# Kernel tuning notes

Measured on AMD Instinct MI355X. Metric: run time of the kernel, lower is better.

Reference implementation:

```python
import jax, jax.numpy as jnp
import numpy as np
from jax import lax

B, L, E = 2, 2048, 1024          # batch, seq_len, embed_dim
NL = 2                            # n_layers
DI = 2 * E                        # d_inner (expand=2)
DS = 16                           # d_state
DC = 4                            # d_conv
DTR = (E + 15) // 16              # dt_rank = ceil(d_model/16) = 64


def setup_inputs() -> dict:
    key = jax.random.key(0)
    ks = jax.random.split(key, 12)
    s = 0.02
    inp = {
        "x": jax.random.normal(ks[0], (B, L, E), jnp.float32),
        "pos_embed": jax.random.normal(ks[1], (L, E), jnp.float32) * s,
        "in_proj_w": jax.random.normal(ks[2], (NL, 2 * DI, E), jnp.float32) * s,
        "conv_w": jax.random.normal(ks[3], (NL, DI, DC), jnp.float32) * s,
        "conv_b": jnp.zeros((NL, DI), jnp.float32),
        "x_proj_w": jax.random.normal(ks[4], (NL, DTR + 2 * DS, DI), jnp.float32) * s,
        "dt_proj_w": jax.random.normal(ks[5], (NL, DI, DTR), jnp.float32) * s,
        "dt_bias": jax.random.normal(ks[6], (NL, DI), jnp.float32) * 0.1,
        "A_log": jnp.broadcast_to(jnp.log(jnp.arange(1, DS + 1, dtype=jnp.float32)), (NL, DI, DS)) + 0.0,
        "D_skip": jnp.ones((NL, DI), jnp.float32),
        "out_proj_w": jax.random.normal(ks[7], (NL, E, DI), jnp.float32) * s,
        "norm_w": jnp.ones((NL, E), jnp.float32),
    }
    return inp


def _rmsnorm(x, w, eps=1e-6):
    return x * lax.rsqrt(jnp.mean(x * x, axis=-1, keepdims=True) + eps) * w


def _mamba(h, in_w, cw, cb, xw, dtw, dtb, A_log, Dp, ow):
    # h: (B, L, E)
    xz = jnp.einsum("ble,de->bld", h, in_w)          # (B, L, 2*DI)
    xc, z = jnp.split(xz, 2, axis=-1)                 # each (B, L, DI)
    # causal depthwise conv1d (kernel DC)
    xp = jnp.pad(xc, ((0, 0), (DC - 1, 0), (0, 0)))
    xconv = cb
    acc = jnp.zeros_like(xc)
    for k in range(DC):
        acc = acc + cw[:, k] * xp[:, k:k + xc.shape[1], :]
    xc = jax.nn.silu(acc + cb)
    # input-dependent SSM params
    x_dbl = jnp.einsum("bld,rd->blr", xc, xw)         # (B, L, DTR+2*DS)
    dt, Bm, C = jnp.split(x_dbl, [DTR, DTR + DS], axis=-1)
    delta = jax.nn.softplus(jnp.einsum("blr,dr->bld", dt, dtw) + dtb)  # (B, L, DI)
    A = -jnp.exp(A_log)                               # (DI, DS)

    def step(hst, inp):
        d, bm, c, u = inp                             # (B,DI),(B,DS),(B,DS),(B,DI)
        hst = jnp.exp(d[..., None] * A) * hst + (d * u)[..., None] * bm[:, None, :]
        y = jnp.einsum("bdn,bn->bd", hst, c)
        return hst, y

    h0 = jnp.zeros((h.shape[0], DI, DS), h.dtype)
    _, ys = lax.scan(step, h0, (delta.swapaxes(0, 1), Bm.swapaxes(0, 1),
                                C.swapaxes(0, 1), xc.swapaxes(0, 1)))
    y = ys.swapaxes(0, 1) + xc * Dp                   # (B, L, DI)
    y = y * jax.nn.silu(z)
    return jnp.einsum("bld,ed->ble", y, ow)


def reference(x, pos_embed, in_proj_w, conv_w, conv_b, x_proj_w, dt_proj_w,
              dt_bias, A_log, D_skip, out_proj_w, norm_w):
    h = x + pos_embed[None, :x.shape[1]]
    for i in range(in_proj_w.shape[0]):
        y = _mamba(h, in_proj_w[i], conv_w[i], conv_b[i], x_proj_w[i],
                   dt_proj_w[i], dt_bias[i], A_log[i], D_skip[i], out_proj_w[i])
        h = _rmsnorm(y + h, norm_w[i])
    return h
```

## Files before the change

### kernel.cpp

```cpp
#include <hip/hip_runtime.h>

#define B_   2
#define L_   2048
#define E_   1024
#define NL_  2
#define DI_  2048
#define DS_  16
#define DC_  4
#define DTR_ 64
#define NXD_ 96
#define M_   (B_ * L_)
#define NCH_ 64
#define LC_  32

typedef __attribute__((ext_vector_type(8))) short bf16x8;
typedef __attribute__((ext_vector_type(4))) float f32x4;

__device__ __forceinline__ float bf2f(unsigned short u) {
    return __uint_as_float(((unsigned)u) << 16);
}
__device__ __forceinline__ unsigned short f2bf(float f) {
    unsigned u = __float_as_uint(f);
    u += 0x7fff + ((u >> 16) & 1);
    return (unsigned short)(u >> 16);
}

#define LOG2E_ 1.44269504f
#define LN2_   0.69314718f

__device__ __forceinline__ float sigmoidf_(float x) {
    return __builtin_amdgcn_rcpf(1.f + __builtin_amdgcn_exp2f(-x * LOG2E_));
}
__device__ __forceinline__ float softplusf_(float x) {
    float e = __builtin_amdgcn_exp2f(x * LOG2E_);
    float s = LN2_ * __builtin_amdgcn_logf(1.f + e);
    return x > 15.f ? x : s;
}
__device__ __forceinline__ float expf_(float x) {
    return __builtin_amdgcn_exp2f(x * LOG2E_);
}
__device__ __forceinline__ float ldin(const void* p, size_t i, int isbf) {
    return isbf ? bf2f(((const unsigned short*)p)[i]) : ((const float*)p)[i];
}
__device__ __forceinline__ void gld_lds16(const unsigned short* g, unsigned short* l) {
    __builtin_amdgcn_global_load_lds(
        (const __attribute__((address_space(1))) unsigned int*)g,
        (__attribute__((address_space(3))) unsigned int*)l, 16, 0, 0);
}

__device__ __forceinline__ void expvec(int fast, float dv, const float* a2, float* e) {
    if (fast) {
        float p1 = __builtin_amdgcn_exp2f(dv * a2[0]);
        float p2 = p1 * p1, p4 = p2 * p2, p8 = p4 * p4;
        e[0] = p1;        e[1] = p2;        e[2] = p2 * p1;   e[3] = p4;
        e[4] = p4 * p1;   e[5] = p4 * p2;   e[6] = e[5] * p1; e[7] = p8;
        e[8] = p8 * p1;   e[9] = p8 * p2;   e[10] = e[9] * p1; e[11] = p8 * p4;
        e[12] = e[11] * p1; e[13] = e[11] * p2; e[14] = e[13] * p1; e[15] = p8 * p8;
    } else {
#pragma unroll
        for (int n = 0; n < 16; ++n) e[n] = __builtin_amdgcn_exp2f(dv * a2[n]);
    }
}

__global__ __launch_bounds__(256) void detect_kernel(const unsigned* __restrict__ x,
                                                     int* __restrict__ flags)
{
    __shared__ int cnt;
    if (threadIdx.x == 0) cnt = 0;
    __syncthreads();
    unsigned v = x[threadIdx.x];
    int e = (v >> 7) & 0xFF;
    if (e >= 90 && e <= 140) atomicAdd(&cnt, 1);
    __syncthreads();
    if (threadIdx.x == 0) {
        flags[0] = (cnt >= 192) ? 1 : 0;
        flags[1] = 1;
        flags[2] = 1;
    }
}

__global__ __launch_bounds__(256) void chk_alog(
    const void* __restrict__ alog, int* __restrict__ flags)
{
    int isbf = flags[0];
    int i = blockIdx.x * 256 + threadIdx.x;
    int layer = i / (DI_ * DS_);
    int n = i & (DS_ - 1);
    float a  = -expf_(ldin(alog, i, isbf));
    float a0 = -expf_(ldin(alog, i - n, isbf));
    float want = (n + 1) * a0;
    if (fabsf(a - want) > 0.02f * fabsf(want))
        atomicAnd(&flags[1 + layer], 0);
}

#define WB_IN_  0
#define WB_XW_  4194304
#define WB_DTW_ 4456448
#define WB_OW_  4587520
#define WB_TOT_ 6684672
__global__ __launch_bounds__(256) void cvt_layer_kernel(
    const void* __restrict__ inw, const void* __restrict__ xw,
    const void* __restrict__ dtw, const void* __restrict__ ow,
    int layer, unsigned short* __restrict__ wbuf, const int* __restrict__ flag)
{
    int isbf = *flag;
    int i = blockIdx.x * 256 + threadIdx.x;
    unsigned short v;
    if (i < WB_XW_) {
        v = isbf ? ((const unsigned short*)inw)[(size_t)layer * 2 * DI_ * E_ + i]
                 : f2bf(((const float*)inw)[(size_t)layer * 2 * DI_ * E_ + i]);
    } else if (i < WB_DTW_) {
        int j = i - WB_XW_; int r = j >> 11, k = j & (DI_ - 1);
        v = (r < NXD_)
          ? (isbf ? ((const unsigned short*)xw)[(size_t)layer * NXD_ * DI_ + (size_t)r * DI_ + k]
                  : f2bf(((const float*)xw)[(size_t)layer * NXD_ * DI_ + (size_t)r * DI_ + k]))
          : (unsigned short)0;
    } else if (i < WB_OW_) {
        int j = i - WB_DTW_;
        v = isbf ? ((const unsigned short*)dtw)[(size_t)layer * DI_ * DTR_ + j]
                 : f2bf(((const float*)dtw)[(size_t)layer * DI_ * DTR_ + j]);
    } else {
        int j = i - WB_OW_;
        v = isbf ? ((const unsigned short*)ow)[(size_t)layer * E_ * DI_ + j]
                 : f2bf(((const float*)ow)[(size_t)layer * E_ * DI_ + j]);
    }
    wbuf[i] = v;
}

__global__ __launch_bounds__(256) void add_pos_kernel(
    const void* __restrict__ x, const void* __restrict__ pos,
    float* __restrict__ h, unsigned short* __restrict__ h16,
    const int* __restrict__ flag)
{
    int isbf = *flag;
    int i = blockIdx.x * 256 + threadIdx.x;
    float v = ldin(x, i, isbf) + ldin(pos, i & (L_ * E_ - 1), isbf);
    h[i] = v;
    h16[i] = f2bf(v);
}

__global__ __launch_bounds__(256) void gemm_mfma(
    const unsigned short* __restrict__ A, int lda,
    const unsigned short* __restrict__ W, int ldw,
    void* __restrict__ C, int ldc, int Ksplit, size_t cSliceStride,
    const void* __restrict__ bias, size_t boff,
    void* __restrict__ C2, int ep, const int* __restrict__ flag)
{
    __shared__ unsigned short As[128 * 64];
    __shared__ unsigned short Bs[128 * 64];
    int tid = threadIdx.x;
    int lane = tid & 63, w = tid >> 6;
    int m0 = blockIdx.x * 128, n0 = blockIdx.y * 128;
    int wm = (w >> 1) * 64, wn = (w & 1) * 64;
    int col = lane & 15, quad = lane >> 4;
    int kstart = blockIdx.z * Ksplit;

    f32x4 acc[4][4];
#pragma unroll
    for (int i = 0; i < 4; ++i)
#pragma unroll
        for (int j = 0; j < 4; ++j)
            acc[i][j] = (f32x4){0.f, 0.f, 0.f, 0.f};

    for (int kt = kstart; kt < kstart + Ksplit; kt += 64) {
#pragma unroll
        for (int i = 0; i < 4; ++i) {
            int seg = i * 4 + w;
            int q = seg * 64 + lane;
            int r = q >> 3, cd = q & 7;
            int cs = cd ^ (r & 7);
            gld_lds16(A + (size_t)(m0 + r) * lda + kt + cs * 8, &As[seg * 512]);
            gld_lds16(W + (size_t)(n0 + r) * ldw + kt + cs * 8, &Bs[seg * 512]);
        }
        __syncthreads();
#pragma unroll
        for (int ks = 0; ks < 2; ++ks) {
            bf16x8 af[4], bfr[4];
#pragma unroll
            for (int t = 0; t < 4; ++t) {
                int rowA = wm + t * 16 + col;
                int ca = ks * 4 + quad;
                af[t]  = *(const bf16x8*)&As[rowA * 64 + ((ca ^ (rowA & 7)) * 8)];
                int rowB = wn + t * 16 + col;
                bfr[t] = *(const bf16x8*)&Bs[rowB * 64 + ((ca ^ (rowB & 7)) * 8)];
            }
#pragma unroll
            for (int tm = 0; tm < 4; ++tm)
#pragma unroll
                for (int tn = 0; tn < 4; ++tn)
                    acc[tm][tn] = __builtin_amdgcn_mfma_f32_16x16x32_bf16(
                        af[tm], bfr[tn], acc[tm][tn], 0, 0, 0);
        }
        __syncthreads();
    }

    int isbf = flag ? *flag : 1;
    float* Cp = (float*)C + (size_t)blockIdx.z * cSliceStride;
#pragma unroll
    for (int tm = 0; tm < 4; ++tm)
#pragma unroll
        for (int tn = 0; tn < 4; ++tn)
#pragma unroll
            for (int rg = 0; rg < 4; ++rg) {
                int gm = m0 + wm + tm * 16 + quad * 4 + rg;
                int gn = n0 + wn + tn * 16 + col;
                float v = acc[tm][tn][rg];
                if (ep == 0) {
                    Cp[(size_t)gm * ldc + gn] = v;
                } else {
                    v = softplusf_(v + ldin(bias, boff + gn, isbf));
                    ((unsigned short*)C)[(size_t)gm * ldc + gn] = f2bf(v);
                }
            }
}

#define G8_NT (E_ / 32)
__global__ __launch_bounds__(512) void gemm_inproj8(
    const unsigned short* __restrict__ A,
    const unsigned short* __restrict__ W,
    unsigned short* __restrict__ Cx,
    unsigned short* __restrict__ Cz)
{
    __shared__ unsigned short lds[65536];
    int tid = threadIdx.x;
    int lane = tid & 63, w = tid >> 6;
    int wr = w >> 2, wc = w & 3;
    int col = lane & 15, quad = lane >> 4;

    int flat = blockIdx.y * 16 + blockIdx.x;
    int nn = (flat & 7) * 32 + (flat >> 3);
    int cch = nn >> 5, wi = nn & 31;
    int bx = (cch & 3) * 4 + (wi & 3);
    int by = (cch >> 2) * 8 + (wi >> 2);
    int m0 = bx * 256, n0 = by * 256;

    const unsigned short* srcA = A + (size_t)(m0 + (lane & 15)) * E_ + (lane >> 4) * 8;
    const unsigned short* srcW = W + (size_t)(n0 + (lane & 15)) * E_ + (lane >> 4) * 8;

    f32x4 acc[8][4];
#pragma unroll
    for (int i = 0; i < 8; ++i)
#pragma unroll
        for (int j = 0; j < 4; ++j)
            acc[i][j] = (f32x4){0.f, 0.f, 0.f, 0.f};

#pragma unroll
    for (int tp = 0; tp < 3; ++tp) {
#pragma unroll
        for (int s = 0; s < 2; ++s) {
            int seg = s * 8 + w;
            gld_lds16(srcA + (size_t)seg * 16 * E_ + tp * 32, &lds[tp * 16384 + seg * 512]);
            gld_lds16(srcW + (size_t)seg * 16 * E_ + tp * 32, &lds[tp * 16384 + 8192 + seg * 512]);
        }
    }

    for (int t = 0; t < G8_NT; ++t) {
        if (t < G8_NT - 2)       asm volatile("s_waitcnt vmcnt(8)" ::: "memory");
        else if (t == G8_NT - 2) asm volatile("s_waitcnt vmcnt(4)" ::: "memory");
        else                     asm volatile("s_waitcnt vmcnt(0)" ::: "memory");
        __builtin_amdgcn_s_barrier();

        int cb = (t & 3) * 16384;
        int sb = ((t + 3) & 3) * 16384;
        int kt = (t + 3) * 32;

        if ((t + 3) < G8_NT) {
#pragma unroll
            for (int s = 0; s < 2; ++s) {
                int seg = s * 8 + w;
                gld_lds16(srcA + (size_t)seg * 16 * E_ + kt, &lds[sb + seg * 512]);
                gld_lds16(srcW + (size_t)seg * 16 * E_ + kt, &lds[sb + 8192 + seg * 512]);
            }
        }

        bf16x8 bfr[4], af[8];
#pragma unroll
        for (int tn = 0; tn < 4; ++tn)
            bfr[tn] = *(const bf16x8*)&lds[cb + 8192 + (wc * 4 + tn) * 512 + quad * 128 + col * 8];
#pragma unroll
        for (int t8 = 0; t8 < 8; ++t8)
            af[t8] = *(const bf16x8*)&lds[cb + (wr * 8 + t8) * 512 + quad * 128 + col * 8];

        __builtin_amdgcn_s_setprio(1);
#pragma unroll
        for (int tm = 0; tm < 8; ++tm)
#pragma unroll
            for (int tn = 0; tn < 4; ++tn)
                acc[tm][tn] = __builtin_amdgcn_mfma_f32_16x16x32_bf16(
                    af[tm], bfr[tn], acc[tm][tn], 0, 0, 0);
        __builtin_amdgcn_s_setprio(0);
    }

    unsigned short* dst = (n0 < DI_) ? Cx : Cz;
    int nb = (n0 < DI_) ? n0 : n0 - DI_;
#pragma unroll
    for (int tm = 0; tm < 8; ++tm)
#pragma unroll
        for (int tn = 0; tn < 4; ++tn)
#pragma unroll
            for (int rg = 0; rg < 4; ++rg) {
                int gm = m0 + wr * 128 + tm * 16 + quad * 4 + rg;
                int gn = nb + wc * 64 + tn * 16 + col;
                dst[(size_t)gm * DI_ + gn] = f2bf(acc[tm][tn][rg]);
            }
}

__global__ __launch_bounds__(256) void xproj_reduce(
    const float* __restrict__ part, float* __restrict__ xdbl,
    unsigned short* __restrict__ dt16)
{
    int i = blockIdx.x * 256 + threadIdx.x;
    int r = i >> 7, c = i & 127;
    float v = 0.f;
#pragma unroll
    for (int s = 0; s < 8; ++s) v += part[(size_t)s * (M_ * 128) + i];
    if (c < NXD_) xdbl[(size_t)r * NXD_ + c] = v;
    if (c < DTR_) dt16[(size_t)r * DTR_ + c] = f2bf(v);
}

__global__ __launch_bounds__(256) void conv_prep(
    const void* __restrict__ cw, size_t cwoff, const void* __restrict__ cb,
    size_t cboff, float* __restrict__ cwT, float* __restrict__ cbF,
    const int* __restrict__ flag)
{
    int isbf = *flag;
    int d = blockIdx.x * 256 + threadIdx.x;
#pragma unroll
    for (int k = 0; k < DC_; ++k)
        cwT[k * DI_ + d] = ldin(cw, cwoff + (size_t)d * DC_ + k, isbf);
    cbF[d] = ldin(cb, cboff + d, isbf);
}

#define CT_ 4
__global__ __launch_bounds__(256) void conv_silu_v(
    const unsigned short* __restrict__ xcr16, const float* __restrict__ cwT,
    const float* __restrict__ cbF, unsigned short* __restrict__ xc16)
{
    int g = blockIdx.x;
    int bl0 = g * CT_;
    int l0 = bl0 & (L_ - 1);
    int d = threadIdx.x * 8;

    float w[DC_][8], bias[8];
#pragma unroll
    for (int k = 0; k < DC_; ++k) {
        *(float4*)&w[k][0] = *(const float4*)&cwT[k * DI_ + d];
        *(float4*)&w[k][4] = *(const float4*)&cwT[k * DI_ + d + 4];
    }
    *(float4*)&bias[0] = *(const float4*)&cbF[d];
    *(float4*)&bias[4] = *(const float4*)&cbF[d + 4];

    float xr[DC_ - 1 + CT_][8];
#pragma unroll
    for (int r = 0; r < DC_ - 1 + CT_; ++r) {
        int l = l0 - (DC_ - 1) + r;
        if (l >= 0) {
            bf16x8 v = *(const bf16x8*)&xcr16[(size_t)(bl0 - (DC_ - 1) + r) * DI_ + d];
#pragma unroll
            for (int j = 0; j < 8; ++j) xr[r][j] = bf2f((unsigned short)v[j]);
        } else {
#pragma unroll
            for (int j = 0; j < 8; ++j) xr[r][j] = 0.f;
        }
    }

#pragma unroll
    for (int t = 0; t < CT_; ++t) {
        float acc[8];
#pragma unroll
        for (int j = 0; j < 8; ++j) acc[j] = bias[j];
#pragma unroll
        for (int k = 0; k < DC_; ++k)
#pragma unroll
            for (int j = 0; j < 8; ++j)
                acc[j] = fmaf(w[k][j], xr[t + k][j], acc[j]);
        bf16x8 ov;
#pragma unroll
        for (int j = 0; j < 8; ++j) {
            float s = acc[j] * sigmoidf_(acc[j]);
            ov[j] = (short)f2bf(s);
        }
        *(bf16x8*)&xc16[(size_t)(bl0 + t) * DI_ + d] = ov;
    }
}

__global__ __launch_bounds__(256) void scan_part1(
    const unsigned short* __restrict__ dl16, const unsigned short* __restrict__ xc16,
    const float* __restrict__ xdbl,
    const void* __restrict__ A_log, size_t aoff,
    float* __restrict__ sumdbuf, float* __restrict__ scrS,
    const int* __restrict__ flags, int layer)
{
    int isbf = flags[0], fast = flags[1 + layer];
    __shared__ float bs[LC_][16];
    int c = blockIdx.y;
    int b = blockIdx.x >> 3;
    int d = ((blockIdx.x & 7) << 8) + threadIdx.x;
    for (int i = threadIdx.x; i < LC_ * 16; i += 256) {
        int l = i >> 4, n = i & 15;
        bs[l][n] = xdbl[((size_t)b * L_ + c * LC_ + l) * NXD_ + DTR_ + n];
    }
    __syncthreads();
    float a2[16];
#pragma unroll
    for (int n = 0; n < 16; ++n)
        a2[n] = -expf_(ldin(A_log, aoff + (size_t)d * DS_ + n, isbf)) * LOG2E_;
    float s[16] = {};
    float sumd = 0.f;
    const unsigned short* dp = dl16 + ((size_t)b * L_ + c * LC_) * DI_ + d;
    const unsigned short* up = xc16 + ((size_t)b * L_ + c * LC_) * DI_ + d;
    for (int l = 0; l < LC_; ++l) {
        float dv = bf2f(dp[(size_t)l * DI_]);
        float u  = bf2f(up[(size_t)l * DI_]);
        sumd += dv;
        float dvu = dv * u;
        float e[16];
        expvec(fast, dv, a2, e);
        float4 b0 = *(const float4*)&bs[l][0];
        float4 b1 = *(const float4*)&bs[l][4];
        float4 b2 = *(const float4*)&bs[l][8];
        float4 b3 = *(const float4*)&bs[l][12];
        float bv[16] = {b0.x,b0.y,b0.z,b0.w, b1.x,b1.y,b1.z,b1.w,
                        b2.x,b2.y,b2.z,b2.w, b3.x,b3.y,b3.z,b3.w};
#pragma unroll
        for (int n = 0; n < 16; ++n)
            s[n] = fmaf(e[n], s[n], dvu * bv[n]);
    }
    int g = b * DI_ + d;
    sumdbuf[(size_t)c * (B_ * DI_) + g] = sumd;
    size_t base = ((size_t)c * (B_ * DI_) + g) * 16;
#pragma unroll
    for (int q = 0; q < 4; ++q)
        *(float4*)&scrS[base + q * 4] =
            make_float4(s[q*4], s[q*4+1], s[q*4+2], s[q*4+3]);
}

__global__ __launch_bounds__(256) void scan_combine(
    const float* __restrict__ sumdbuf, float* __restrict__ scrS,
    const void* __restrict__ A_log, size_t aoff, const int* __restrict__ flags)
{
    int isbf = flags[0];
    int t = blockIdx.x * 256 + threadIdx.x;
    int g = t >> 4, n = t & 15;
    int d = g & (DI_ - 1);
    float a2 = -expf_(ldin(A_log, aoff + (size_t)d * DS_ + n, isbf)) * LOG2E_;
    float sd[NCH_], sl[NCH_];
#pragma unroll
    for (int c = 0; c < NCH_; ++c) {
        sd[c] = sumdbuf[(size_t)c * (B_ * DI_) + g];
        sl[c] = scrS[(size_t)c * (B_ * DI_ * 16) + t];
    }
    float s = 0.f;
#pragma unroll
    for (int c = 0; c < NCH_; ++c) {
        float P = __builtin_amdgcn_exp2f(a2 * sd[c]);
        float nxt = fmaf(P, s, sl[c]);
        scrS[(size_t)c * (B_ * DI_ * 16) + t] = s;
        s = nxt;
    }
}

__global__ __launch_bounds__(256) void scan_part2(
    const unsigned short* __restrict__ dl16, unsigned short* __restrict__ xc16,
    const float* __restrict__ xdbl, const unsigned short* __restrict__ z,
    const void* __restrict__ A_log, size_t aoff,
    const void* __restrict__ Dskip, size_t doff,
    const float* __restrict__ scrS, const int* __restrict__ flags, int layer)
{
    int isbf = flags[0], fast = flags[1 + layer];
    __shared__ float bs[LC_][32];
    int c = blockIdx.y;
    int b = blockIdx.x >> 3;
    int d = ((blockIdx.x & 7) << 8) + threadIdx.x;
    for (int i = threadIdx.x; i < LC_ * 32; i += 256) {
        int l = i >> 5, n = i & 31;
        bs[l][n] = xdbl[((size_t)b * L_ + c * LC_ + l) * NXD_ + DTR_ + n];
    }
    __syncthreads();
    float a2[16];
#pragma unroll
    for (int n = 0; n < 16; ++n)
        a2[n] = -expf_(ldin(A_log, aoff + (size_t)d * DS_ + n, isbf)) * LOG2E_;
    float Dv = ldin(Dskip, doff + d, isbf);
    int g = b * DI_ + d;
    size_t sbase = ((size_t)c * (B_ * DI_) + g) * 16;
    float s[16];
#pragma unroll
    for (int q = 0; q < 4; ++q) {
        float4 sv = *(const float4*)&scrS[sbase + q * 4];
        s[q*4] = sv.x; s[q*4+1] = sv.y; s[q*4+2] = sv.z; s[q*4+3] = sv.w;
    }

    const unsigned short* dp = dl16 + ((size_t)b * L_ + c * LC_) * DI_ + d;
    unsigned short* up = xc16 + ((size_t)b * L_ + c * LC_) * DI_ + d;
    const unsigned short* zp = z + ((size_t)b * L_ + c * LC_) * DI_ + d;
    for (int l = 0; l < LC_; ++l) {
        float dv = bf2f(dp[(size_t)l * DI_]);
        float u  = bf2f(up[(size_t)l * DI_]);
        float dvu = dv * u;
        float e[16];
        expvec(fast, dv, a2, e);
        float4 b0 = *(const float4*)&bs[l][0];
        float4 b1 = *(const float4*)&bs[l][4];
        float4 b2 = *(const float4*)&bs[l][8];
        float4 b3 = *(const float4*)&bs[l][12];
        float4 c0 = *(const float4*)&bs[l][16];
        float4 c1 = *(const float4*)&bs[l][20];
        float4 c2 = *(const float4*)&bs[l][24];
        float4 c3 = *(const float4*)&bs[l][28];
        float bv[16] = {b0.x,b0.y,b0.z,b0.w, b1.x,b1.y,b1.z,b1.w,
                        b2.x,b2.y,b2.z,b2.w, b3.x,b3.y,b3.z,b3.w};
        float cv[16] = {c0.x,c0.y,c0.z,c0.w, c1.x,c1.y,c1.z,c1.w,
                        c2.x,c2.y,c2.z,c2.w, c3.x,c3.y,c3.z,c3.w};
        float y = 0.f;
#pragma unroll
        for (int n = 0; n < 16; ++n) {
            s[n] = fmaf(e[n], s[n], dvu * bv[n]);
            y = fmaf(s[n], cv[n], y);
        }
        float zv = bf2f(zp[(size_t)l * DI_]);
        up[(size_t)l * DI_] = f2bf((y + u * Dv) * (zv * sigmoidf_(zv)));
    }
}

__global__ __launch_bounds__(256) void rmsnorm_kernel(
    const float* __restrict__ y0, const float* __restrict__ y1,
    float* __restrict__ h, unsigned short* __restrict__ h16,
    const void* __restrict__ nw, size_t nwoff, void* __restrict__ out,
    int write_out, const int* __restrict__ flag)
{
    int isbf = *flag;
    __shared__ float red[4];
    int row = blockIdx.x;
    float* hp = h + (size_t)row * E_;
    float v[4]; float ss = 0.f;
#pragma unroll
    for (int i = 0; i < 4; ++i) {
        int e = threadIdx.x + i * 256;
        size_t idx = (size_t)row * E_ + e;
        v[i] = y0[idx] + y1[idx] + hp[e];
        ss += v[i] * v[i];
    }
#pragma unroll
    for (int off = 1; off < 64; off <<= 1) ss += __shfl_xor(ss, off, 64);
    if ((threadIdx.x & 63) == 0) red[threadIdx.x >> 6] = ss;
    __syncthreads();
    ss = red[0] + red[1] + red[2] + red[3];
    float scale = rsqrtf(ss * (1.f / E_) + 1e-6f);
#pragma unroll
    for (int i = 0; i < 4; ++i) {
        int e = threadIdx.x + i * 256;
        float hv = v[i] * scale * ldin(nw, nwoff + e, isbf);
        hp[e] = hv;
        h16[(size_t)row * E_ + e] = f2bf(hv);
        if (write_out) {
            size_t oi = (size_t)row * E_ + e;
            if (isbf) ((unsigned short*)out)[oi] = f2bf(hv);
            else      ((float*)out)[oi] = hv;
        }
    }
}

extern "C" void kernel_launch(void* const* d_in, const int* in_sizes, int n_in,
                              void* d_out, int out_size, void* d_ws, size_t ws_size,
                              hipStream_t stream)
{
    const void* x    = d_in[0];
    const void* pos  = d_in[1];
    const void* inw  = d_in[2];
    const void* cw   = d_in[3];
    const void* cb   = d_in[4];
    const void* xw   = d_in[5];
    const void* dtw  = d_in[6];
    const void* dtb  = d_in[7];
    const void* alog = d_in[8];
    const void* dsk  = d_in[9];
    const void* ow   = d_in[10];
    const void* nw   = d_in[11];

    float* ws = (float*)d_ws;
    float* h      = ws;
    unsigned short* h16  = (unsigned short*)(ws + 4194304);
    unsigned short* z16  = (unsigned short*)(ws + 6291456);
    unsigned short* xc16 = (unsigned short*)(ws + 10485760);
    float* D      = ws + 14680064;
    float* R      = ws + 23068672;
    float* xdbl   = ws + 27262976;
    unsigned short* dt16 = (unsigned short*)(ws + 27656192);
    float* sumd   = ws + 27787264;
    unsigned short* wbuf = (unsigned short*)(ws + 28049408);
    int* flags    = (int*)(ws + 31391744);

    unsigned short* xcr16 = (unsigned short*)R;
    float* xp_part = R;
    float* scrS    = R;
    unsigned short* dl16 = (unsigned short*)D;
    float* yout0 = D;
    float* yout1 = D + (size_t)M_ * E_;
    float* cwT = sumd;
    float* cbF = sumd + DC_ * DI_;

    detect_kernel<<<1, 256, 0, stream>>>((const unsigned*)x, flags);
    chk_alog<<<NL_ * DI_ * DS_ / 256, 256, 0, stream>>>(alog, flags);
    add_pos_kernel<<<M_ * E_ / 256, 256, 0, stream>>>(x, pos, h, h16, flags);

    for (int layer = 0; layer < NL_; ++layer) {
        cvt_layer_kernel<<<WB_TOT_ / 256, 256, 0, stream>>>(
            inw, xw, dtw, ow, layer, wbuf, flags);
        conv_prep<<<DI_ / 256, 256, 0, stream>>>(
            cw, (size_t)layer * DI_ * DC_, cb, (size_t)layer * DI_, cwT, cbF, flags);

        gemm_inproj8<<<dim3(M_ / 256, 2 * DI_ / 256, 1), 512, 0, stream>>>(
            h16, wbuf + WB_IN_, xcr16, z16);
        conv_silu_v<<<M_ / CT_, 256, 0, stream>>>(xcr16, cwT, cbF, xc16);
        gemm_mfma<<<dim3(M_ / 128, 1, 8), 256, 0, stream>>>(
            xc16, DI_, wbuf + WB_XW_, DI_, xp_part, 128, DI_ / 8, (size_t)M_ * 128,
            nullptr, 0, nullptr, 0, flags);
        xproj_reduce<<<M_ * 128 / 256, 256, 0, stream>>>(xp_part, xdbl, dt16);
        gemm_mfma<<<dim3(M_ / 128, DI_ / 128, 1), 256, 0, stream>>>(
            dt16, DTR_, wbuf + WB_DTW_, DTR_, dl16, DI_, DTR_, 0,
            dtb, (size_t)layer * DI_, nullptr, 2, flags);
        scan_part1<<<dim3(B_ * DI_ / 256, NCH_), 256, 0, stream>>>(
            dl16, xc16, xdbl, alog, (size_t)layer * DI_ * DS_, sumd, scrS, flags, layer);
        scan_combine<<<B_ * DI_ * DS_ / 256, 256, 0, stream>>>(
            sumd, scrS, alog, (size_t)layer * DI_ * DS_, flags);
        scan_part2<<<dim3(B_ * DI_ / 256, NCH_), 256, 0, stream>>>(
            dl16, xc16, xdbl, z16, alog, (size_t)layer * DI_ * DS_,
            dsk, (size_t)layer * DI_, scrS, flags, layer);
        gemm_mfma<<<dim3(M_ / 128, E_ / 128, 2), 256, 0, stream>>>(
            xc16, DI_, wbuf + WB_OW_, DI_, yout0, E_, DI_ / 2, (size_t)M_ * E_,
            nullptr, 0, nullptr, 0, flags);
        rmsnorm_kernel<<<M_, 256, 0, stream>>>(
            yout0, yout1, h, h16, nw, (size_t)layer * E_, d_out,
            layer == NL_ - 1 ? 1 : 0, flags);
    }
}
```

Before: 567.6 us.

## Read bf16 weights directly and re-pipeline in-proj GEMM with half-phase staging

When inputs are already bf16, the weight-conversion kernel now skips copying the in_proj, dt_proj and out_proj weights, and the GEMMs read the original weight arrays directly. This removes redundant copy traffic. The in-projection GEMM mainloop is rewritten to use a 64-wide K tile with double-buffered LDS. Each tile is processed in eight phases that interleave inline-asm ds_read_b128 fragment loads, global-to-LDS staging and MFMA bursts, each phase separated by explicit barriers and waitcnts. This aims to overlap memory and compute more finely, at the cost of more barriers and fragile hand-coded wait counts.

```diff
diff --git a/kernel.cpp b/kernel.cpp
--- a/kernel.cpp
+++ b/kernel.cpp
@@ -47,6 +47,11 @@
         (const __attribute__((address_space(1))) unsigned int*)g,
         (__attribute__((address_space(3))) unsigned int*)l, 16, 0, 0);
 }
+__device__ __forceinline__ bf16x8 ds_read128_(unsigned byteoff) {
+    bf16x8 r;
+    asm volatile("ds_read_b128 %0, %1" : "=&v"(r) : "v"(byteoff));
+    return r;
+}
 
 __device__ __forceinline__ void expvec(int fast, float dv, const float* a2, float* e) {
     if (fast) {
@@ -105,6 +110,7 @@
 {
     int isbf = *flag;
     int i = blockIdx.x * 256 + threadIdx.x;
+    if (isbf && (i < WB_XW_ || i >= WB_DTW_)) return;
     unsigned short v;
     if (i < WB_XW_) {
         v = isbf ? ((const unsigned short*)inw)[(size_t)layer * 2 * DI_ * E_ + i]
@@ -144,10 +150,13 @@
     const unsigned short* __restrict__ W, int ldw,
     void* __restrict__ C, int ldc, int Ksplit, size_t cSliceStride,
     const void* __restrict__ bias, size_t boff,
-    void* __restrict__ C2, int ep, const int* __restrict__ flag)
+    void* __restrict__ C2, int ep, const int* __restrict__ flag,
+    const unsigned short* __restrict__ Worig)
 {
     __shared__ unsigned short As[128 * 64];
     __shared__ unsigned short Bs[128 * 64];
+    int isbf = flag ? *flag : 1;
+    const unsigned short* Wp = (Worig && isbf) ? Worig : W;
     int tid = threadIdx.x;
     int lane = tid & 63, w = tid >> 6;
     int m0 = blockIdx.x * 128, n0 = blockIdx.y * 128;
@@ -170,7 +179,7 @@
             int r = q >> 3, cd = q & 7;
             int cs = cd ^ (r & 7);
             gld_lds16(A + (size_t)(m0 + r) * lda + kt + cs * 8, &As[seg * 512]);
-            gld_lds16(W + (size_t)(n0 + r) * ldw + kt + cs * 8, &Bs[seg * 512]);
+            gld_lds16(Wp + (size_t)(n0 + r) * ldw + kt + cs * 8, &Bs[seg * 512]);
         }
         __syncthreads();
 #pragma unroll
@@ -194,7 +203,6 @@
         __syncthreads();
     }
 
-    int isbf = flag ? *flag : 1;
     float* Cp = (float*)C + (size_t)blockIdx.z * cSliceStride;
 #pragma unroll
     for (int tm = 0; tm < 4; ++tm)
@@ -214,14 +222,57 @@
             }
 }
 
-#define G8_NT (E_ / 32)
+template <int KS, int MH, int RB, int CHK>
+__device__ __forceinline__ void g8_phase(
+    unsigned baseA, unsigned baseB,
+    bf16x8 (&af)[4], bf16x8 (&bfr)[4], f32x4 (&acc)[8][4],
+    int doStage, int st_t, int st_isB, int st_ks,
+    const unsigned short* srcA, const unsigned short* srcW,
+    unsigned short* ldsb, int w)
+{
+    if (RB) {
+#pragma unroll
+        for (int j = 0; j < 4; ++j)
+            bfr[j] = ds_read128_(baseB + j * 2048 + KS * 1024);
+    }
+#pragma unroll
+    for (int f = 0; f < 4; ++f)
+        af[f] = ds_read128_(baseA + MH * 8192 + f * 2048 + KS * 1024);
+    if (doStage) {
+        const unsigned short* s0 = (st_isB ? srcW : srcA)
+            + (size_t)w * 16 * E_ + st_t * 64 + st_ks * 32;
+        unsigned short* d0 = ldsb + (st_t & 1) * 32768 + st_isB * 16384
+            + w * 1024 + st_ks * 512;
+        gld_lds16(s0, d0);
+        gld_lds16(s0 + (size_t)8 * 16 * E_, d0 + 8 * 1024);
+    }
+    __builtin_amdgcn_s_barrier();
+    asm volatile("s_waitcnt lgkmcnt(0)" ::: "memory");
+    __builtin_amdgcn_sched_barrier(0);
+    __builtin_amdgcn_s_setprio(1);
+#pragma unroll
+    for (int f = 0; f < 4; ++f)
+#pragma unroll
+        for (int j = 0; j < 4; ++j)
+            acc[MH * 4 + f][j] = __builtin_amdgcn_mfma_f32_16x16x32_bf16(
+                af[f], bfr[j], acc[MH * 4 + f][j], 0, 0, 0);
+    __builtin_amdgcn_s_setprio(0);
+    if (CHK == 8) { asm volatile("s_waitcnt vmcnt(8)" ::: "memory"); __builtin_amdgcn_sched_barrier(0); }
+    if (CHK == 4) { asm volatile("s_waitcnt vmcnt(4)" ::: "memory"); __builtin_amdgcn_sched_barrier(0); }
+    if (CHK == 0) { asm volatile("s_waitcnt vmcnt(0)"  ::: "memory"); __builtin_amdgcn_sched_barrier(0); }
+    __builtin_amdgcn_s_barrier();
+}
+
 __global__ __launch_bounds__(512) void gemm_inproj8(
     const unsigned short* __restrict__ A,
-    const unsigned short* __restrict__ W,
+    const unsigned short* __restrict__ Wbuf,
+    const unsigned short* __restrict__ Worig,
+    const int* __restrict__ flag,
     unsigned short* __restrict__ Cx,
     unsigned short* __restrict__ Cz)
 {
     __shared__ unsigned short lds[65536];
+    const unsigned short* W = (*flag) ? Worig : Wbuf;
     int tid = threadIdx.x;
     int lane = tid & 63, w = tid >> 6;
     int wr = w >> 2, wc = w & 3;
@@ -237,59 +288,48 @@
     const unsigned short* srcA = A + (size_t)(m0 + (lane & 15)) * E_ + (lane >> 4) * 8;
     const unsigned short* srcW = W + (size_t)(n0 + (lane & 15)) * E_ + (lane >> 4) * 8;
 
+    unsigned baseA0 = (unsigned)(wr * 8 * 2048 + quad * 256 + col * 16);
+    unsigned baseB0 = (unsigned)(32768 + wc * 4 * 2048 + quad * 256 + col * 16);
+    unsigned baseA1 = baseA0 + 65536, baseB1 = baseB0 + 65536;
+
     f32x4 acc[8][4];
 #pragma unroll
     for (int i = 0; i < 8; ++i)
 #pragma unroll
         for (int j = 0; j < 4; ++j)
             acc[i][j] = (f32x4){0.f, 0.f, 0.f, 0.f};
-
-#pragma unroll
-    for (int tp = 0; tp < 3; ++tp) {
-#pragma unroll
-        for (int s = 0; s < 2; ++s) {
-            int seg = s * 8 + w;
-            gld_lds16(srcA + (size_t)seg * 16 * E_ + tp * 32, &lds[tp * 16384 + seg * 512]);
-            gld_lds16(srcW + (size_t)seg * 16 * E_ + tp * 32, &lds[tp * 16384 + 8192 + seg * 512]);
-        }
-    }
-
-    for (int t = 0; t < G8_NT; ++t) {
-        if (t < G8_NT - 2)       asm volatile("s_waitcnt vmcnt(8)" ::: "memory");
-        else if (t == G8_NT - 2) asm volatile("s_waitcnt vmcnt(4)" ::: "memory");
-        else                     asm volatile("s_waitcnt vmcnt(0)" ::: "memory");
-        __builtin_amdgcn_s_barrier();
-
-        int cb = (t & 3) * 16384;
-        int sb = ((t + 3) & 3) * 16384;
-        int kt = (t + 3) * 32;
-
-        if ((t + 3) < G8_NT) {
-#pragma unroll
-            for (int s = 0; s < 2; ++s) {
-                int seg = s * 8 + w;
-                gld_lds16(srcA + (size_t)seg * 16 * E_ + kt, &lds[sb + seg * 512]);
-                gld_lds16(srcW + (size_t)seg * 16 * E_ + kt, &lds[sb + 8192 + seg * 512]);
-            }
-        }
-
-        bf16x8 bfr[4], af[8];
-#pragma unroll
-        for (int tn = 0; tn < 4; ++tn)
-            bfr[tn] = *(const bf16x8*)&lds[cb + 8192 + (wc * 4 + tn) * 512 + quad * 128 + col * 8];
-#pragma unroll
-        for (int t8 = 0; t8 < 8; ++t8)
-            af[t8] = *(const bf16x8*)&lds[cb + (wr * 8 + t8) * 512 + quad * 128 + col * 8];
-
-        __builtin_amdgcn_s_setprio(1);
-#pragma unroll
-        for (int tm = 0; tm < 8; ++tm)
-#pragma unroll
-            for (int tn = 0; tn < 4; ++tn)
-                acc[tm][tn] = __builtin_amdgcn_mfma_f32_16x16x32_bf16(
-                    af[tm], bfr[tn], acc[tm][tn], 0, 0, 0);
-        __builtin_amdgcn_s_setprio(0);
-    }
+    bf16x8 af[4], bfr[4];
+
+#define G8STAGE(t_, isB_, ks_) { \
+    const unsigned short* s0 = ((isB_) ? srcW : srcA) + (size_t)w * 16 * E_ + (t_) * 64 + (ks_) * 32; \
+    unsigned short* d0 = lds + ((t_) & 1) * 32768 + (isB_) * 16384 + w * 1024 + (ks_) * 512; \
+    gld_lds16(s0, d0); gld_lds16(s0 + (size_t)8 * 16 * E_, d0 + 8 * 1024); }
+
+    G8STAGE(0, 0, 0) G8STAGE(0, 1, 0) G8STAGE(0, 0, 1) G8STAGE(0, 1, 1)
+    G8STAGE(1, 0, 0) G8STAGE(1, 1, 0)
+    asm volatile("s_waitcnt vmcnt(8)" ::: "memory");
+    __builtin_amdgcn_sched_barrier(0);
+    __builtin_amdgcn_s_barrier();
+
+    for (int i = 0; i < 7; ++i) {
+        int t1 = 2 * i + 1, t2 = 2 * i + 2, t3 = 2 * i + 3;
+        g8_phase<0,0,1,-1>(baseA0, baseB0, af, bfr, acc, 1, t1, 0, 1, srcA, srcW, lds, w);
+        g8_phase<0,1,0, 8>(baseA0, baseB0, af, bfr, acc, 1, t1, 1, 1, srcA, srcW, lds, w);
+        g8_phase<1,0,1,-1>(baseA0, baseB0, af, bfr, acc, 1, t2, 0, 0, srcA, srcW, lds, w);
+        g8_phase<1,1,0, 8>(baseA0, baseB0, af, bfr, acc, 1, t2, 1, 0, srcA, srcW, lds, w);
+        g8_phase<0,0,1,-1>(baseA1, baseB1, af, bfr, acc, 1, t2, 0, 1, srcA, srcW, lds, w);
+        g8_phase<0,1,0, 8>(baseA1, baseB1, af, bfr, acc, 1, t2, 1, 1, srcA, srcW, lds, w);
+        g8_phase<1,0,1,-1>(baseA1, baseB1, af, bfr, acc, 1, t3, 0, 0, srcA, srcW, lds, w);
+        g8_phase<1,1,0, 8>(baseA1, baseB1, af, bfr, acc, 1, t3, 1, 0, srcA, srcW, lds, w);
+    }
+    g8_phase<0,0,1,-1>(baseA0, baseB0, af, bfr, acc, 1, 15, 0, 1, srcA, srcW, lds, w);
+    g8_phase<0,1,0, 8>(baseA0, baseB0, af, bfr, acc, 1, 15, 1, 1, srcA, srcW, lds, w);
+    g8_phase<1,0,1,-1>(baseA0, baseB0, af, bfr, acc, 0, 0, 0, 0, srcA, srcW, lds, w);
+    g8_phase<1,1,0, 4>(baseA0, baseB0, af, bfr, acc, 0, 0, 0, 0, srcA, srcW, lds, w);
+    g8_phase<0,0,1,-1>(baseA1, baseB1, af, bfr, acc, 0, 0, 0, 0, srcA, srcW, lds, w);
+    g8_phase<0,1,0, 0>(baseA1, baseB1, af, bfr, acc, 0, 0, 0, 0, srcA, srcW, lds, w);
+    g8_phase<1,0,1,-1>(baseA1, baseB1, af, bfr, acc, 0, 0, 0, 0, srcA, srcW, lds, w);
+    g8_phase<1,1,0,-1>(baseA1, baseB1, af, bfr, acc, 0, 0, 0, 0, srcA, srcW, lds, w);
 
     unsigned short* dst = (n0 < DI_) ? Cx : Cz;
     int nb = (n0 < DI_) ? n0 : n0 - DI_;
@@ -303,6 +343,7 @@
                 int gn = nb + wc * 64 + tn * 16 + col;
                 dst[(size_t)gm * DI_ + gn] = f2bf(acc[tm][tn][rg]);
             }
+#undef G8STAGE
 }
 
 __global__ __launch_bounds__(256) void xproj_reduce(
@@ -605,21 +646,25 @@
     add_pos_kernel<<<M_ * E_ / 256, 256, 0, stream>>>(x, pos, h, h16, flags);
 
     for (int layer = 0; layer < NL_; ++layer) {
+        const unsigned short* inws = (const unsigned short*)inw + (size_t)layer * 2 * DI_ * E_;
+        const unsigned short* dtws = (const unsigned short*)dtw + (size_t)layer * DI_ * DTR_;
+        const unsigned short* ows  = (const unsigned short*)ow  + (size_t)layer * E_ * DI_;
+
         cvt_layer_kernel<<<WB_TOT_ / 256, 256, 0, stream>>>(
             inw, xw, dtw, ow, layer, wbuf, flags);
         conv_prep<<<DI_ / 256, 256, 0, stream>>>(
             cw, (size_t)layer * DI_ * DC_, cb, (size_t)layer * DI_, cwT, cbF, flags);
 
         gemm_inproj8<<<dim3(M_ / 256, 2 * DI_ / 256, 1), 512, 0, stream>>>(
-            h16, wbuf + WB_IN_, xcr16, z16);
+            h16, wbuf + WB_IN_, inws, flags, xcr16, z16);
         conv_silu_v<<<M_ / CT_, 256, 0, stream>>>(xcr16, cwT, cbF, xc16);
         gemm_mfma<<<dim3(M_ / 128, 1, 8), 256, 0, stream>>>(
             xc16, DI_, wbuf + WB_XW_, DI_, xp_part, 128, DI_ / 8, (size_t)M_ * 128,
-            nullptr, 0, nullptr, 0, flags);
+            nullptr, 0, nullptr, 0, flags, nullptr);
         xproj_reduce<<<M_ * 128 / 256, 256, 0, stream>>>(xp_part, xdbl, dt16);
         gemm_mfma<<<dim3(M_ / 128, DI_ / 128, 1), 256, 0, stream>>>(
             dt16, DTR_, wbuf + WB_DTW_, DTR_, dl16, DI_, DTR_, 0,
-            dtb, (size_t)layer * DI_, nullptr, 2, flags);
+            dtb, (size_t)layer * DI_, nullptr, 2, flags, dtws);
         scan_part1<<<dim3(B_ * DI_ / 256, NCH_), 256, 0, stream>>>(
             dl16, xc16, xdbl, alog, (size_t)layer * DI_ * DS_, sumd, scrS, flags, layer);
         scan_combine<<<B_ * DI_ * DS_ / 256, 256, 0, stream>>>(
@@ -629,7 +674,7 @@
             dsk, (size_t)layer * DI_, scrS, flags, layer);
         gemm_mfma<<<dim3(M_ / 128, E_ / 128, 2), 256, 0, stream>>>(
             xc16, DI_, wbuf + WB_OW_, DI_, yout0, E_, DI_ / 2, (size_t)M_ * E_,
-            nullptr, 0, nullptr, 0, flags);
+            nullptr, 0, nullptr, 0, flags, ows);
         rmsnorm_kernel<<<M_, 256, 0, stream>>>(
             yout0, yout1, h, h16, nw, (size_t)layer * E_, d_out,
             layer == NL_ - 1 ? 1 : 0, flags);
```

Measured after the change: 568.5 us. No clear change (+0.2%).
